# Optimization experiments

Hardware: AMD Instinct MI355X
Metric: run time of the kernel (lower is better)

## Reference

```python
import jax, jax.numpy as jnp
import numpy as np

EPS = 1e-5

def conv2d(x, w, stride=1, pad=0, groups=1):
    return jax.lax.conv_general_dilated(
        x, w, (stride, stride), [(pad, pad), (pad, pad)],
        feature_group_count=groups,
        dimension_numbers=('NCHW', 'OIHW', 'NCHW'))

def prelu(x, a):
    return jnp.where(x > 0, x, a[None, :, None, None] * x)

def batchnorm(x, g, b):
    # training-mode BN: batch statistics over N,H,W (biased variance, as torch)
    m = jnp.mean(x, axis=(0, 2, 3), keepdims=True)
    v = jnp.var(x, axis=(0, 2, 3), keepdims=True)
    xhat = (x - m) * jax.lax.rsqrt(v + EPS)
    return xhat * g[None, :, None, None] + b[None, :, None, None]

def setup_inputs() -> dict:
    key = jax.random.key(0)
    ks = jax.random.split(key, 8)
    C_in, C_out, stride = 128, 256, 2
    x = jax.random.normal(ks[0], (32, C_in, 56, 56), dtype=jnp.float32)
    w1 = jax.random.normal(ks[1], (C_out, C_in, 1, 1), dtype=jnp.float32) * 0.05
    w_dw = jax.random.normal(ks[2], (C_out, 1, 3, 3), dtype=jnp.float32) * 0.1
    w3 = jax.random.normal(ks[3], (C_out, C_out, 1, 1), dtype=jnp.float32) * 0.05
    w_adj = jax.random.normal(ks[4], (C_out, C_in, 1, 1), dtype=jnp.float32) * 0.05
    a_init = jnp.full((C_out,), 0.25, dtype=jnp.float32)  # PReLU init
    ones = jnp.ones((C_out,), dtype=jnp.float32)
    zeros = jnp.zeros((C_out,), dtype=jnp.float32)
    return {
        'x': x,
        'w1': w1, 'a1': a_init, 'g1': ones, 'b1': zeros,
        'w_dw': w_dw, 'a2': a_init, 'g2': ones, 'b2': zeros,
        'w3': w3, 'a3': a_init, 'g3': ones, 'b3': zeros,
        'w_adj': w_adj,
    }

def reference(x, w1, a1, g1, b1, w_dw, a2, g2, b2, w3, a3, g3, b3, w_adj):
    stride, C_out = 2, w_dw.shape[0]
    residual = conv2d(x, w_adj, stride=stride)  # full-precision shortcut
    xs = jnp.sign(x)
    # binary 1x1 conv (sign(x) already signed; sign is idempotent)
    out = conv2d(jnp.sign(xs), jnp.sign(w1))
    out = batchnorm(prelu(out, a1), g1, b1)
    # binary depthwise 3x3, stride, pad 1
    out = conv2d(jnp.sign(out), jnp.sign(w_dw), stride=stride, pad=1, groups=C_out)
    out = batchnorm(prelu(out, a2), g2, b2)
    # binary 1x1 conv
    out = conv2d(jnp.sign(out), jnp.sign(w3))
    out = batchnorm(prelu(out, a3), g3, b3)
    return out + residual
```

## Files before the change

### kernel.cpp

```cpp
#include <hip/hip_runtime.h>
#include <stdint.h>

#define NB   32
#define CIN  128
#define COUT 256
#define HH   56
#define WW   56
#define S1   (HH*WW)
#define HO   28
#define WO   28
#define S2   (HO*WO)
#define NS1  (NB*S1)
#define NS2  (NB*S2)
#define TOT2 (NS2*COUT)
#define EPSV 1e-5f

constexpr size_t OFF_XBITS = 0;
constexpr size_t OFF_WB1   = OFF_XBITS + (size_t)NS1*8*4;
constexpr size_t OFF_WB3   = OFF_WB1 + 256*8*4;
constexpr size_t OFF_WDW   = OFF_WB3 + 256*16*4;
constexpr size_t OFF_ACC   = OFF_WDW + 4096;
constexpr size_t OFF_WBADJ = OFF_ACC + 3*256*4*sizeof(int);
constexpr size_t OFF_XG    = OFF_WBADJ + (size_t)COUT*CIN*2;
constexpr size_t OFF_OUT1  = OFF_XG + (size_t)NS2*CIN*2;
constexpr size_t OFF_OUT2  = OFF_OUT1 + (size_t)NS1*COUT;
constexpr size_t OFF_XB2   = OFF_OUT2 + (size_t)TOT2;
constexpr size_t OFF_OUT3  = OFF_XB2 + (size_t)NS2*16*4;

typedef __attribute__((ext_vector_type(8))) short bf16x8;
typedef __attribute__((ext_vector_type(4))) float f32x4;

__device__ __forceinline__ uint32_t f2bf(float v) {
  uint32_t u = __float_as_uint(v);
  return (u + 0x7fffu + ((u >> 16) & 1u)) >> 16;
}

__device__ __forceinline__ void bn_finalize(const int* __restrict__ acc4,
                                            float a, float g, float b, float inv_ns,
                                            float& sc, float& sh) {
  float ps = (float)acc4[0];
  float ng = (float)acc4[1];
  float pq = (float)acc4[2];
  float nq = (float)acc4[3];
  float mean = (ps + a*ng) * inv_ns;
  float ex2  = (pq + a*a*nq) * inv_ns;
  float var  = ex2 - mean*mean;
  float rs   = rsqrtf(var + EPSV);
  sc = rs * g;
  sh = b - mean * sc;
}

__global__ __launch_bounds__(256) void packx_kernel(
    const float* __restrict__ x, uint32_t* __restrict__ xbits,
    uint32_t* __restrict__ xg,
    const float* __restrict__ w1, const float* __restrict__ w3,
    const float* __restrict__ wdw, const float* __restrict__ wadj,
    uint32_t* __restrict__ wb1, uint32_t* __restrict__ wb3,
    int8_t* __restrict__ wdws, uint32_t* __restrict__ wbadj,
    int* __restrict__ accbase) {
  int wdx = blockIdx.y;
  if (wdx == 0 && blockIdx.x < 256 && threadIdx.x < 64) {
    int co = blockIdx.x;
    int l  = threadIdx.x;
    if (l < 12) {
      int set = l >> 2, k = l & 3;
      accbase[set*1024 + co*4 + k] = 0;
    }
    for (int h = 0; h < 2; ++h) {
      float v = w1[(size_t)co*CIN + h*64 + l];
      unsigned long long bp = __ballot(v > 0.f);
      unsigned long long bn = __ballot(v < 0.f);
      if (l == 0) {
        wb1[co*8 + 2*h    ] = (uint32_t)bp;
        wb1[co*8 + 2*h + 1] = (uint32_t)(bp >> 32);
        wb1[co*8 + 4 + 2*h    ] = (uint32_t)bn;
        wb1[co*8 + 4 + 2*h + 1] = (uint32_t)(bn >> 32);
      }
    }
    for (int h = 0; h < 4; ++h) {
      float v = w3[(size_t)co*COUT + h*64 + l];
      unsigned long long bp = __ballot(v > 0.f);
      unsigned long long bn = __ballot(v < 0.f);
      if (l == 0) {
        wb3[co*16 + 2*h    ] = (uint32_t)bp;
        wb3[co*16 + 2*h + 1] = (uint32_t)(bp >> 32);
        wb3[co*16 + 8 + 2*h    ] = (uint32_t)bn;
        wb3[co*16 + 8 + 2*h + 1] = (uint32_t)(bn >> 32);
      }
    }
    if (l < 9) {
      float v = wdw[co*9 + l];
      wdws[co*9 + l] = (int8_t)((v > 0.f) - (v < 0.f));
    }
    {
      float v0 = wadj[(size_t)co*CIN + 2*l];
      float v1 = wadj[(size_t)co*CIN + 2*l + 1];
      wbadj[co*64 + l] = f2bf(v0) | (f2bf(v1) << 16);
    }
  }

  int m = blockIdx.x*256 + threadIdx.x;
  int n = m / S1, hw = m % S1;
  size_t base = ((size_t)n*CIN + wdx*32)*S1 + hw;
  uint32_t p = 0, q = 0;
  uint32_t bv[16];
  #pragma unroll
  for (int j = 0; j < 32; ++j) {
    float v = x[base + (size_t)j*S1];
    p |= (uint32_t)(v > 0.f) << j;
    q |= (uint32_t)(v < 0.f) << j;
    uint32_t b = f2bf(v);
    if (j & 1) bv[j >> 1] |= b << 16; else bv[j >> 1] = b;
  }
  xbits[(size_t)m*8 + wdx    ] = p;
  xbits[(size_t)m*8 + 4 + wdx] = q;
  int h = hw / WW, w = hw % WW;
  if (((h | w) & 1) == 0) {
    int m2 = n*S2 + (h >> 1)*WO + (w >> 1);
    uint4* dst = (uint4*)(xg + (size_t)m2*64 + wdx*16);
    dst[0] = make_uint4(bv[0],  bv[1],  bv[2],  bv[3]);
    dst[1] = make_uint4(bv[4],  bv[5],  bv[6],  bv[7]);
    dst[2] = make_uint4(bv[8],  bv[9],  bv[10], bv[11]);
    dst[3] = make_uint4(bv[12], bv[13], bv[14], bv[15]);
  }
}

__global__ __launch_bounds__(256) void conv1_kernel(
    const uint32_t* __restrict__ xb, const uint32_t* __restrict__ wb,
    int8_t* __restrict__ out1, int* __restrict__ accum1) {
  int tid = threadIdx.x;
  int qm = blockIdx.x*256 + tid;
  int m0 = qm*4;
  int n  = m0 / S1;
  int hw0 = m0 - n*S1;
  int co0 = blockIdx.y * 8;

  const uint4* xw = (const uint4*)(xb + (size_t)m0*8);
  uint4 xp0 = xw[0], xq0 = xw[1];
  uint4 xp1 = xw[2], xq1 = xw[3];
  uint4 xp2 = xw[4], xq2 = xw[5];
  uint4 xp3 = xw[6], xq3 = xw[7];

  uint32_t nzw = (xp0.x|xq0.x)&(xp0.y|xq0.y)&(xp0.z|xq0.z)&(xp0.w|xq0.w)
               & (xp1.x|xq1.x)&(xp1.y|xq1.y)&(xp1.z|xq1.z)&(xp1.w|xq1.w)
               & (xp2.x|xq2.x)&(xp2.y|xq2.y)&(xp2.z|xq2.z)&(xp2.w|xq2.w)
               & (xp3.x|xq3.x)&(xp3.y|xq3.y)&(xp3.z|xq3.z)&(xp3.w|xq3.w);
  bool allnz = (nzw == 0xffffffffu);

  __shared__ int sl[256][17];
  __shared__ int sW[4][16];
  uint32_t res[8];
  int stp[8], stn[8], stpq[8], stnq[8];

  #pragma unroll
  for (int j = 0; j < 8; ++j) {
    const uint32_t* w8 = wb + (size_t)(co0 + j)*8;
    uint32_t w0 = w8[0], w1 = w8[1], w2 = w8[2], w3 = w8[3];
    int A0,A1,A2,A3;
#define XORDOT(i,A) A = 128 - 2*(__popc(xp##i.x^w0)+__popc(xp##i.y^w1)+__popc(xp##i.z^w2)+__popc(xp##i.w^w3));
    XORDOT(0,A0) XORDOT(1,A1) XORDOT(2,A2) XORDOT(3,A3)
#undef XORDOT
    if (!allnz) {
#define ZCORR(i,A) { \
      uint32_t z0 = ~(xp##i.x|xq##i.x), z1 = ~(xp##i.y|xq##i.y); \
      uint32_t z2 = ~(xp##i.z|xq##i.z), z3 = ~(xp##i.w|xq##i.w); \
      A += 2*(__popc(z0&w0)+__popc(z1&w1)+__popc(z2&w2)+__popc(z3&w3)) \
         - (__popc(z0)+__popc(z1)+__popc(z2)+__popc(z3)); }
      ZCORR(0,A0) ZCORR(1,A1) ZCORR(2,A2) ZCORR(3,A3)
#undef ZCORR
    }
    if (A0 > 127) A0 = 127;
    if (A1 > 127) A1 = 127;
    if (A2 > 127) A2 = 127;
    if (A3 > 127) A3 = 127;
    res[j] = (uint32_t)(uint8_t)A0 | ((uint32_t)(uint8_t)A1 << 8)
           | ((uint32_t)(uint8_t)A2 << 16) | ((uint32_t)(uint8_t)A3 << 24);
    int ps = 0, ns = 0, pq = 0, nq = 0;
#define STAT(A) if (A > 0) { ps += A; pq += A*A; } else { ns += A; nq += A*A; }
    STAT(A0) STAT(A1) STAT(A2) STAT(A3)
#undef STAT
    stp[j] = ps; stn[j] = ns; stpq[j] = pq; stnq[j] = nq;
  }

  #pragma unroll
  for (int j = 0; j < 4; ++j) {
    sl[tid][j*4+0] = stp[j];  sl[tid][j*4+1] = stn[j];
    sl[tid][j*4+2] = stpq[j]; sl[tid][j*4+3] = stnq[j];
  }
  __syncthreads();

  #pragma unroll
  for (int j = 0; j < 8; ++j)
    *(uint32_t*)(out1 + (size_t)(n*COUT + co0 + j)*S1 + hw0) = res[j];

  int s16 = tid & 15, ch = tid >> 4;
  {
    int part = 0;
    #pragma unroll
    for (int i = 0; i < 16; ++i) part += sl[ch + 16*i][s16];
    part += __shfl_xor(part, 16);
    part += __shfl_xor(part, 32);
    if ((tid & 63) < 16) sW[tid >> 6][s16] = part;
  }
  __syncthreads();
  if (tid < 16) {
    int tot = sW[0][tid] + sW[1][tid] + sW[2][tid] + sW[3][tid];
    atomicAdd(&accum1[co0*4 + tid], tot);
  }

  #pragma unroll
  for (int j = 0; j < 4; ++j) {
    sl[tid][j*4+0] = stp[4+j];  sl[tid][j*4+1] = stn[4+j];
    sl[tid][j*4+2] = stpq[4+j]; sl[tid][j*4+3] = stnq[4+j];
  }
  __syncthreads();
  {
    int part = 0;
    #pragma unroll
    for (int i = 0; i < 16; ++i) part += sl[ch + 16*i][s16];
    part += __shfl_xor(part, 16);
    part += __shfl_xor(part, 32);
    if ((tid & 63) < 16) sW[tid >> 6][s16] = part;
  }
  __syncthreads();
  if (tid < 16) {
    int tot = sW[0][tid] + sW[1][tid] + sW[2][tid] + sW[3][tid];
    atomicAdd(&accum1[co0*4 + 16 + tid], tot);
  }
}

#define DW_SLABS 8
#define DW_RB    68
__global__ __launch_bounds__(256) void dw_kernel(
    const int8_t* __restrict__ out1, const int8_t* __restrict__ wdws,
    const int* __restrict__ acc1, const float* __restrict__ a1,
    const float* __restrict__ g1, const float* __restrict__ b1,
    int8_t* __restrict__ out2, int* __restrict__ accum2) {
  __shared__ int8_t sl[DW_SLABS][57][DW_RB];
  __shared__ int sTp[DW_SLABS], sTn[DW_SLABS], sAcc[DW_SLABS][4];
  int tid = threadIdx.x;
  int nc0 = blockIdx.x * DW_SLABS;
  int co0 = nc0 & (COUT-1);

  int* slw = (int*)&sl[0][0][0];
  #pragma unroll
  for (int i = tid; i < DW_SLABS*57*DW_RB/4; i += 256) slw[i] = 0;
  if (tid < DW_SLABS) { sTp[tid] = 128; sTn[tid] = -129; }
  if (tid < DW_SLABS*4) sAcc[tid >> 2][tid & 3] = 0;
  __syncthreads();

  {
    int slab = tid >> 5;
    int co = co0 + slab;
    float av = a1[co], sc, sh;
    bn_finalize(acc1 + co*4, av, g1[co], b1[co], 1.f/NS1, sc, sh);
    int tp = 128, tn = -129;
    int v0 = -128 + (tid & 31)*8;
    #pragma unroll
    for (int k = 0; k < 8; ++k) {
      int v = v0 + k;
      float f = (float)v;
      float pr = f > 0.f ? f : av*f;
      float tv = pr*sc + sh;
      if (tv > 0.f && v < tp) tp = v;
      if (tv < 0.f && v > tn) tn = v;
    }
    atomicMin(&sTp[slab], tp);
    atomicMax(&sTn[slab], tn);
  }
  __syncthreads();

  for (int i = tid; i < DW_SLABS*784; i += 256) {
    int slab = i / 784;
    int d    = i - slab*784;
    int ih   = d / 14;
    int iwd  = d - ih*14;
    int Tp = sTp[slab], Tn = sTn[slab];
    uint32_t v4 = ((const uint32_t*)(out1 + (size_t)(nc0 + slab)*S1))[d];
    uint32_t s4 = 0;
    #pragma unroll
    for (int k = 0; k < 4; ++k) {
      int v = (int)(int8_t)(v4 >> (8*k));
      int s = (v >= Tp) - (v <= Tn);
      s4 |= (uint32_t)(s & 0xff) << (8*k);
    }
    *(uint32_t*)&sl[slab][ih + 1][4 + 4*iwd] = s4;
  }
  __syncthreads();

  int psum = 0, nsum = 0, psq = 0, nsq = 0;
  int slabD = tid / HO;
  if (tid < DW_SLABS*HO) {
    int ho   = tid - slabD*HO;
    int nc = nc0 + slabD;
    int co = co0 + slabD;
    int wv[9];
    #pragma unroll
    for (int k = 0; k < 9; ++k) wv[k] = wdws[co*9 + k];
    const uint32_t* r0 = (const uint32_t*)&sl[slabD][2*ho    ][4];
    const uint32_t* r1 = (const uint32_t*)&sl[slabD][2*ho + 1][4];
    const uint32_t* r2 = (const uint32_t*)&sl[slabD][2*ho + 2][4];
    uint32_t* o32 = (uint32_t*)(out2 + (size_t)nc*S2 + ho*WO);
    int c0 = 0, c1 = 0, c2 = 0;
    uint32_t obuf = 0;
    #pragma unroll
    for (int q = 0; q < 14; ++q) {
      uint32_t d0 = r0[q], d1 = r1[q], d2 = r2[q];
      int s00=(int)(int8_t)d0, s01=(int)(int8_t)(d0>>8), s02=(int)(int8_t)(d0>>16), s03=(int)(int8_t)(d0>>24);
      int s10=(int)(int8_t)d1, s11=(int)(int8_t)(d1>>8), s12=(int)(int8_t)(d1>>16), s13=(int)(int8_t)(d1>>24);
      int s20=(int)(int8_t)d2, s21=(int)(int8_t)(d2>>8), s22=(int)(int8_t)(d2>>16), s23=(int)(int8_t)(d2>>24);
      int a0 = c0*wv[0] + s00*wv[1] + s01*wv[2]
             + c1*wv[3] + s10*wv[4] + s11*wv[5]
             + c2*wv[6] + s20*wv[7] + s21*wv[8];
      int a1v = s01*wv[0] + s02*wv[1] + s03*wv[2]
              + s11*wv[3] + s12*wv[4] + s13*wv[5]
              + s21*wv[6] + s22*wv[7] + s23*wv[8];
      c0 = s03; c1 = s13; c2 = s23;
      if (a0 > 0) { psum += a0; psq += a0*a0; } else { nsum += a0; nsq += a0*a0; }
      if (a1v > 0) { psum += a1v; psq += a1v*a1v; } else { nsum += a1v; nsq += a1v*a1v; }
      if ((q & 1) == 0) {
        obuf = (uint32_t)(a0 & 0xff) | ((uint32_t)(a1v & 0xff) << 8);
      } else {
        obuf |= ((uint32_t)(a0 & 0xff) << 16) | ((uint32_t)(a1v & 0xff) << 24);
        o32[q >> 1] = obuf;
      }
    }
    atomicAdd(&sAcc[slabD][0], psum);
    atomicAdd(&sAcc[slabD][1], nsum);
    atomicAdd(&sAcc[slabD][2], psq);
    atomicAdd(&sAcc[slabD][3], nsq);
  }
  __syncthreads();

  if (tid < DW_SLABS*4) {
    int slab = tid >> 2, k = tid & 3;
    atomicAdd(&accum2[(co0 + slab)*4 + k], sAcc[slab][k]);
  }
}

__global__ __launch_bounds__(256) void pack2_kernel(
    const int8_t* __restrict__ out2, const int* __restrict__ acc2,
    const float* __restrict__ a2, const float* __restrict__ g2,
    const float* __restrict__ b2, uint32_t* __restrict__ xb2) {
  __shared__ int sTp[32], sTn[32];
  int wdx = blockIdx.y;
  if (threadIdx.x < 32) {
    int c = wdx*32 + threadIdx.x;
    float av = a2[c], sc, sh;
    bn_finalize(acc2 + c*4, av, g2[c], b2[c], 1.f/NS2, sc, sh);
    int tp = 10, tn = -10;
    for (int v = -9; v <= 9; ++v) {
      float f = (float)v;
      float pr = f > 0.f ? f : av*f;
      float tv = pr*sc + sh;
      if (tv > 0.f && v < tp) tp = v;
      if (tv < 0.f && v > tn) tn = v;
    }
    sTp[threadIdx.x] = tp; sTn[threadIdx.x] = tn;
  }
  __syncthreads();
  int m = blockIdx.x*256 + threadIdx.x;
  int n = m / S2, hw = m % S2;
  uint32_t p = 0, q = 0;
  #pragma unroll
  for (int j = 0; j < 32; ++j) {
    int c = wdx*32 + j;
    int v = out2[(size_t)(n*COUT + c)*S2 + hw];
    p |= (uint32_t)(v >= sTp[j]) << j;
    q |= (uint32_t)(v <= sTn[j]) << j;
  }
  xb2[(size_t)m*16 + wdx    ] = p;
  xb2[(size_t)m*16 + 8 + wdx] = q;
}

__global__ __launch_bounds__(256) void conv3_kernel(
    const uint32_t* __restrict__ xb2, const uint32_t* __restrict__ wb3,
    int16_t* __restrict__ out3, int* __restrict__ accum3) {
  int tid = threadIdx.x;
  int qm = blockIdx.x*256 + tid;
  int m0 = qm*2;
  int n  = m0 / S2;
  int hw0 = m0 - n*S2;
  int co0 = blockIdx.y * 8;

  const uint4* xw = (const uint4*)(xb2 + (size_t)m0*16);
  uint4 P0a = xw[0], P0b = xw[1], Q0a = xw[2], Q0b = xw[3];
  uint4 P1a = xw[4], P1b = xw[5], Q1a = xw[6], Q1b = xw[7];

  uint32_t nz = (P0a.x|Q0a.x)&(P0a.y|Q0a.y)&(P0a.z|Q0a.z)&(P0a.w|Q0a.w)
              & (P0b.x|Q0b.x)&(P0b.y|Q0b.y)&(P0b.z|Q0b.z)&(P0b.w|Q0b.w)
              & (P1a.x|Q1a.x)&(P1a.y|Q1a.y)&(P1a.z|Q1a.z)&(P1a.w|Q1a.w)
              & (P1b.x|Q1b.x)&(P1b.y|Q1b.y)&(P1b.z|Q1b.z)&(P1b.w|Q1b.w);

  uint32_t res[8];
  if (nz == 0xffffffffu) {
    #pragma unroll
    for (int j = 0; j < 8; ++j) {
      const uint32_t* w = wb3 + (size_t)(co0 + j)*16;
      int s0 = __popc(P0a.x^w[0])+__popc(P0a.y^w[1])+__popc(P0a.z^w[2])+__popc(P0a.w^w[3])
             + __popc(P0b.x^w[4])+__popc(P0b.y^w[5])+__popc(P0b.z^w[6])+__popc(P0b.w^w[7]);
      int s1 = __popc(P1a.x^w[0])+__popc(P1a.y^w[1])+__popc(P1a.z^w[2])+__popc(P1a.w^w[3])
             + __popc(P1b.x^w[4])+__popc(P1b.y^w[5])+__popc(P1b.z^w[6])+__popc(P1b.w^w[7]);
      int a0 = 256 - 2*s0, a1 = 256 - 2*s1;
      res[j] = (uint32_t)(uint16_t)(int16_t)a0 | ((uint32_t)(uint16_t)(int16_t)a1 << 16);
    }
  } else {
    #pragma unroll
    for (int j = 0; j < 8; ++j) {
      const uint32_t* w = wb3 + (size_t)(co0 + j)*16;
      int a0 = __popc(P0a.x&w[0])+__popc(P0a.y&w[1])+__popc(P0a.z&w[2])+__popc(P0a.w&w[3])
             + __popc(P0b.x&w[4])+__popc(P0b.y&w[5])+__popc(P0b.z&w[6])+__popc(P0b.w&w[7])
             + __popc(Q0a.x&w[8])+__popc(Q0a.y&w[9])+__popc(Q0a.z&w[10])+__popc(Q0a.w&w[11])
             + __popc(Q0b.x&w[12])+__popc(Q0b.y&w[13])+__popc(Q0b.z&w[14])+__popc(Q0b.w&w[15])
             - __popc(P0a.x&w[8])-__popc(P0a.y&w[9])-__popc(P0a.z&w[10])-__popc(P0a.w&w[11])
             - __popc(P0b.x&w[12])-__popc(P0b.y&w[13])-__popc(P0b.z&w[14])-__popc(P0b.w&w[15])
             - __popc(Q0a.x&w[0])-__popc(Q0a.y&w[1])-__popc(Q0a.z&w[2])-__popc(Q0a.w&w[3])
             - __popc(Q0b.x&w[4])-__popc(Q0b.y&w[5])-__popc(Q0b.z&w[6])-__popc(Q0b.w&w[7]);
      int a1 = __popc(P1a.x&w[0])+__popc(P1a.y&w[1])+__popc(P1a.z&w[2])+__popc(P1a.w&w[3])
             + __popc(P1b.x&w[4])+__popc(P1b.y&w[5])+__popc(P1b.z&w[6])+__popc(P1b.w&w[7])
             + __popc(Q1a.x&w[8])+__popc(Q1a.y&w[9])+__popc(Q1a.z&w[10])+__popc(Q1a.w&w[11])
             + __popc(Q1b.x&w[12])+__popc(Q1b.y&w[13])+__popc(Q1b.z&w[14])+__popc(Q1b.w&w[15])
             - __popc(P1a.x&w[8])-__popc(P1a.y&w[9])-__popc(P1a.z&w[10])-__popc(P1a.w&w[11])
             - __popc(P1b.x&w[12])-__popc(P1b.y&w[13])-__popc(P1b.z&w[14])-__popc(P1b.w&w[15])
             - __popc(Q1a.x&w[0])-__popc(Q1a.y&w[1])-__popc(Q1a.z&w[2])-__popc(Q1a.w&w[3])
             - __popc(Q1b.x&w[4])-__popc(Q1b.y&w[5])-__popc(Q1b.z&w[6])-__popc(Q1b.w&w[7]);
      res[j] = (uint32_t)(uint16_t)(int16_t)a0 | ((uint32_t)(uint16_t)(int16_t)a1 << 16);
    }
  }

  __shared__ int sl[256][33];
  #pragma unroll
  for (int j = 0; j < 8; ++j) {
    int b0 = (int)(int16_t)(res[j] & 0xffff);
    int b1 = (int)(int16_t)(res[j] >> 16);
    int ps = 0, ns = 0, pq = 0, nq = 0;
    if (b0 > 0) { ps += b0; pq += b0*b0; } else { ns += b0; nq += b0*b0; }
    if (b1 > 0) { ps += b1; pq += b1*b1; } else { ns += b1; nq += b1*b1; }
    sl[tid][j*4+0] = ps; sl[tid][j*4+1] = ns;
    sl[tid][j*4+2] = pq; sl[tid][j*4+3] = nq;
  }
  __syncthreads();

  #pragma unroll
  for (int j = 0; j < 8; ++j)
    *(uint32_t*)(out3 + (size_t)(n*COUT + co0 + j)*S2 + hw0) = res[j];

  int s = tid & 31, g = tid >> 5;
  int part = 0;
  #pragma unroll
  for (int i = 0; i < 32; ++i) part += sl[g + 8*i][s];
  part += __shfl_xor(part, 32);
  __shared__ int sW[4][32];
  if ((tid & 63) < 32) sW[tid >> 6][s] = part;
  __syncthreads();
  if (tid < 32) {
    int tot = sW[0][tid] + sW[1][tid] + sW[2][tid] + sW[3][tid];
    atomicAdd(&accum3[co0*4 + tid], tot);
  }
}

__global__ __launch_bounds__(256) void resfinal_kernel(
    const uint16_t* __restrict__ xg, const uint16_t* __restrict__ wb,
    const int16_t* __restrict__ out3,
    const float* __restrict__ a3, const float* __restrict__ g3,
    const float* __restrict__ b3, const int* __restrict__ acc3,
    float* __restrict__ out) {
  int lane = threadIdx.x & 63;
  int wid  = threadIdx.x >> 6;
  int m0  = blockIdx.x*64 + wid*16;
  int r16 = lane & 15, hi = lane >> 4;
  int koff = hi * 8;

  const bf16x8* arow = (const bf16x8*)(xg + (size_t)(m0 + r16)*CIN + koff);
  bf16x8 af0 = arow[0], af1 = arow[4], af2 = arow[8], af3 = arow[12];

  f32x4 dd[16];
  #pragma unroll
  for (int t = 0; t < 16; ++t) {
    const bf16x8* brow = (const bf16x8*)(wb + (size_t)(t*16 + r16)*CIN + koff);
    f32x4 a = {0.f,0.f,0.f,0.f};
    a = __builtin_amdgcn_mfma_f32_16x16x32_bf16(af0, brow[0],  a, 0,0,0);
    a = __builtin_amdgcn_mfma_f32_16x16x32_bf16(af1, brow[4],  a, 0,0,0);
    a = __builtin_amdgcn_mfma_f32_16x16x32_bf16(af2, brow[8],  a, 0,0,0);
    a = __builtin_amdgcn_mfma_f32_16x16x32_bf16(af3, brow[12], a, 0,0,0);
    dd[t] = a;
  }

  int mrow = m0 + hi*4;
  int n  = mrow / S2;
  int hw = mrow - n*S2;
  #pragma unroll
  for (int t = 0; t < 16; ++t) {
    int co = t*16 + r16;
    float av = a3[co], sc, sh;
    bn_finalize(acc3 + co*4, av, g3[co], b3[co], 1.f/NS2, sc, sh);
    size_t o = ((size_t)n*COUT + co)*S2 + hw;
    #pragma unroll
    for (int r = 0; r < 4; ++r) {
      float f = (float)out3[o + r];
      float pp = f > 0.f ? f : av*f;
      out[o + r] = pp*sc + sh + dd[t][r];
    }
  }
}

extern "C" void kernel_launch(void* const* d_in, const int* in_sizes, int n_in,
                              void* d_out, int out_size, void* d_ws, size_t ws_size,
                              hipStream_t stream) {
  (void)in_sizes; (void)n_in; (void)out_size; (void)ws_size;
  const float* x    = (const float*)d_in[0];
  const float* w1   = (const float*)d_in[1];
  const float* a1   = (const float*)d_in[2];
  const float* g1   = (const float*)d_in[3];
  const float* b1   = (const float*)d_in[4];
  const float* wdw  = (const float*)d_in[5];
  const float* a2   = (const float*)d_in[6];
  const float* g2   = (const float*)d_in[7];
  const float* b2   = (const float*)d_in[8];
  const float* w3   = (const float*)d_in[9];
  const float* a3   = (const float*)d_in[10];
  const float* g3   = (const float*)d_in[11];
  const float* b3   = (const float*)d_in[12];
  const float* wadj = (const float*)d_in[13];
  float* out = (float*)d_out;

  char* ws = (char*)d_ws;
  uint32_t* xbits = (uint32_t*)(ws + OFF_XBITS);
  uint32_t* wb1   = (uint32_t*)(ws + OFF_WB1);
  uint32_t* wb3   = (uint32_t*)(ws + OFF_WB3);
  int8_t*   wdws  = (int8_t*)  (ws + OFF_WDW);
  int*      acc1  = (int*)     (ws + OFF_ACC);
  int*      acc2  = acc1 + 256*4;
  int*      acc3  = acc2 + 256*4;
  uint32_t* wbadj = (uint32_t*)(ws + OFF_WBADJ);
  uint32_t* xg    = (uint32_t*)(ws + OFF_XG);
  int8_t*   out1  = (int8_t*)  (ws + OFF_OUT1);
  int8_t*   out2  = (int8_t*)  (ws + OFF_OUT2);
  uint32_t* xb2   = (uint32_t*)(ws + OFF_XB2);
  int16_t*  out3  = (int16_t*) (ws + OFF_OUT3);

  packx_kernel<<<dim3(NS1/256, 4), 256, 0, stream>>>(
      x, xbits, xg, w1, w3, wdw, wadj, wb1, wb3, wdws, wbadj, acc1);
  conv1_kernel<<<dim3(NS1/1024, 32), 256, 0, stream>>>(xbits, wb1, out1, acc1);
  dw_kernel<<<NB*COUT/DW_SLABS, 256, 0, stream>>>(out1, wdws, acc1, a1, g1, b1, out2, acc2);
  pack2_kernel<<<dim3(NS2/256, 8), 256, 0, stream>>>(out2, acc2, a2, g2, b2, xb2);
  conv3_kernel<<<dim3(NS2/512, 32), 256, 0, stream>>>(xb2, wb3, out3, acc3);
  resfinal_kernel<<<NS2/64, 256, 0, stream>>>(
      (const uint16_t*)xg, (const uint16_t*)wbadj, out3, a3, g3, b3, acc3, out);
}
```

Measured before the change: 110.6 us.

## Store conv3 output pixel-major and precompute BN3 coefficients in shared memory

```diff
diff --git a/kernel.cpp b/kernel.cpp
--- a/kernel.cpp
+++ b/kernel.cpp
@@ -379,8 +379,6 @@
   int tid = threadIdx.x;
   int qm = blockIdx.x*256 + tid;
   int m0 = qm*2;
-  int n  = m0 / S2;
-  int hw0 = m0 - n*S2;
   int co0 = blockIdx.y * 8;
 
   const uint4* xw = (const uint4*)(xb2 + (size_t)m0*16);
@@ -392,7 +390,9 @@
               & (P1a.x|Q1a.x)&(P1a.y|Q1a.y)&(P1a.z|Q1a.z)&(P1a.w|Q1a.w)
               & (P1b.x|Q1b.x)&(P1b.y|Q1b.y)&(P1b.z|Q1b.z)&(P1b.w|Q1b.w);
 
-  uint32_t res[8];
+  uint32_t m0w[4], m1w[4];
+  __shared__ int sl[256][33];
+
   if (nz == 0xffffffffu) {
     #pragma unroll
     for (int j = 0; j < 8; ++j) {
@@ -402,7 +402,18 @@
       int s1 = __popc(P1a.x^w[0])+__popc(P1a.y^w[1])+__popc(P1a.z^w[2])+__popc(P1a.w^w[3])
              + __popc(P1b.x^w[4])+__popc(P1b.y^w[5])+__popc(P1b.z^w[6])+__popc(P1b.w^w[7]);
       int a0 = 256 - 2*s0, a1 = 256 - 2*s1;
-      res[j] = (uint32_t)(uint16_t)(int16_t)a0 | ((uint32_t)(uint16_t)(int16_t)a1 << 16);
+      if ((j & 1) == 0) {
+        m0w[j >> 1] = (uint32_t)(uint16_t)(int16_t)a0;
+        m1w[j >> 1] = (uint32_t)(uint16_t)(int16_t)a1;
+      } else {
+        m0w[j >> 1] |= (uint32_t)(uint16_t)(int16_t)a0 << 16;
+        m1w[j >> 1] |= (uint32_t)(uint16_t)(int16_t)a1 << 16;
+      }
+      int ps = 0, ns = 0, pq = 0, nq = 0;
+      if (a0 > 0) { ps += a0; pq += a0*a0; } else { ns += a0; nq += a0*a0; }
+      if (a1 > 0) { ps += a1; pq += a1*a1; } else { ns += a1; nq += a1*a1; }
+      sl[tid][j*4+0] = ps; sl[tid][j*4+1] = ns;
+      sl[tid][j*4+2] = pq; sl[tid][j*4+3] = nq;
     }
   } else {
     #pragma unroll
@@ -424,26 +435,24 @@
              - __popc(P1b.x&w[12])-__popc(P1b.y&w[13])-__popc(P1b.z&w[14])-__popc(P1b.w&w[15])
              - __popc(Q1a.x&w[0])-__popc(Q1a.y&w[1])-__popc(Q1a.z&w[2])-__popc(Q1a.w&w[3])
              - __popc(Q1b.x&w[4])-__popc(Q1b.y&w[5])-__popc(Q1b.z&w[6])-__popc(Q1b.w&w[7]);
-      res[j] = (uint32_t)(uint16_t)(int16_t)a0 | ((uint32_t)(uint16_t)(int16_t)a1 << 16);
-    }
-  }
-
-  __shared__ int sl[256][33];
-  #pragma unroll
-  for (int j = 0; j < 8; ++j) {
-    int b0 = (int)(int16_t)(res[j] & 0xffff);
-    int b1 = (int)(int16_t)(res[j] >> 16);
-    int ps = 0, ns = 0, pq = 0, nq = 0;
-    if (b0 > 0) { ps += b0; pq += b0*b0; } else { ns += b0; nq += b0*b0; }
-    if (b1 > 0) { ps += b1; pq += b1*b1; } else { ns += b1; nq += b1*b1; }
-    sl[tid][j*4+0] = ps; sl[tid][j*4+1] = ns;
-    sl[tid][j*4+2] = pq; sl[tid][j*4+3] = nq;
-  }
-  __syncthreads();
-
-  #pragma unroll
-  for (int j = 0; j < 8; ++j)
-    *(uint32_t*)(out3 + (size_t)(n*COUT + co0 + j)*S2 + hw0) = res[j];
+      if ((j & 1) == 0) {
+        m0w[j >> 1] = (uint32_t)(uint16_t)(int16_t)a0;
+        m1w[j >> 1] = (uint32_t)(uint16_t)(int16_t)a1;
+      } else {
+        m0w[j >> 1] |= (uint32_t)(uint16_t)(int16_t)a0 << 16;
+        m1w[j >> 1] |= (uint32_t)(uint16_t)(int16_t)a1 << 16;
+      }
+      int ps = 0, ns = 0, pq = 0, nq = 0;
+      if (a0 > 0) { ps += a0; pq += a0*a0; } else { ns += a0; nq += a0*a0; }
+      if (a1 > 0) { ps += a1; pq += a1*a1; } else { ns += a1; nq += a1*a1; }
+      sl[tid][j*4+0] = ps; sl[tid][j*4+1] = ns;
+      sl[tid][j*4+2] = pq; sl[tid][j*4+3] = nq;
+    }
+  }
+  __syncthreads();
+
+  *(uint4*)&out3[(size_t)m0*COUT + co0]       = make_uint4(m0w[0], m0w[1], m0w[2], m0w[3]);
+  *(uint4*)&out3[(size_t)(m0+1)*COUT + co0]   = make_uint4(m1w[0], m1w[1], m1w[2], m1w[3]);
 
   int s = tid & 31, g = tid >> 5;
   int part = 0;
@@ -465,8 +474,17 @@
     const float* __restrict__ a3, const float* __restrict__ g3,
     const float* __restrict__ b3, const int* __restrict__ acc3,
     float* __restrict__ out) {
-  int lane = threadIdx.x & 63;
-  int wid  = threadIdx.x >> 6;
+  __shared__ float scs[256], shs[256], avs[256];
+  int tid = threadIdx.x;
+  {
+    float sc, sh;
+    bn_finalize(acc3 + tid*4, a3[tid], g3[tid], b3[tid], 1.f/NS2, sc, sh);
+    scs[tid] = sc; shs[tid] = sh; avs[tid] = a3[tid];
+  }
+  __syncthreads();
+
+  int lane = tid & 63;
+  int wid  = tid >> 6;
   int m0  = blockIdx.x*64 + wid*16;
   int r16 = lane & 15, hi = lane >> 4;
   int koff = hi * 8;
@@ -492,12 +510,11 @@
   #pragma unroll
   for (int t = 0; t < 16; ++t) {
     int co = t*16 + r16;
-    float av = a3[co], sc, sh;
-    bn_finalize(acc3 + co*4, av, g3[co], b3[co], 1.f/NS2, sc, sh);
+    float av = avs[co], sc = scs[co], sh = shs[co];
     size_t o = ((size_t)n*COUT + co)*S2 + hw;
     #pragma unroll
     for (int r = 0; r < 4; ++r) {
-      float f = (float)out3[o + r];
+      float f = (float)out3[(size_t)(mrow + r)*COUT + co];
       float pp = f > 0.f ? f : av*f;
       out[o + r] = pp*sc + sh + dd[t][r];
     }
```

New measurement: 113.1 us. 1.02x slower.
